# Kernel tuning notes

Measured on AMD Instinct MI355X. Metric: run time of the kernel, lower is better.

Reference implementation:

```python
import jax, jax.numpy as jnp
import numpy as np

INPUT_SIZE = 2048       # init: input_size[-1]
CONF_THRESHOLD = 0.8    # init: conf_threshold
PRED = True             # init: pred -> apply sigmoid


def setup_inputs() -> dict:
    key = jax.random.key(0)
    x = jax.random.normal(key, (1, 133, 512, 512), dtype=jnp.float32)
    return {"x": x}


def reference(x):
    # x: [1, K, H, W]
    heatmaps = jax.nn.sigmoid(x[0]) if PRED else x[0]  # [K, H, W]
    K, H, W = heatmaps.shape
    flat = heatmaps.reshape(K, H * W)
    # Fused masked-argmax over all keypoints in parallel.
    # torch.where returns row-major order, so argmax over thresholded pixels
    # equals the global argmax whenever max confidence exceeds threshold.
    idx = jnp.argmax(flat, axis=1)                      # [K]
    conf = jnp.take_along_axis(flat, idx[:, None], axis=1)[:, 0]  # [K]
    yy = (idx // W).astype(jnp.float32)
    xx = (idx % W).astype(jnp.float32)
    valid = conf > CONF_THRESHOLD                       # [K]
    joints = jnp.where(valid[:, None],
                       jnp.stack([xx, yy, conf], axis=-1),
                       jnp.float32(-1.0))               # [K, 3]
    # Original scales x,y columns for ALL rows (invalid rows become -scale).
    scale = jnp.float32(INPUT_SIZE / W)
    joints = joints.at[:, :2].multiply(scale)
    return joints
```

## Files before the change

### kernel.cpp

```cpp
#include <hip/hip_runtime.h>
#include <math.h>


#define KPTS     133
#define WW       512
#define HW       (512 * 512)
#define NCHUNK   16
#define CHUNK    (HW / NCHUNK)
#define NTHREADS 256
#define V4_PER_T (CHUNK / 4 / NTHREADS)

typedef float floatx4 __attribute__((ext_vector_type(4)));

__device__ __forceinline__ void red(float& bv, unsigned& bi, float v, unsigned i) {
    if (v > bv || (v == bv && i < bi)) { bv = v; bi = i; }
}

__global__ __launch_bounds__(NTHREADS)
void k_phase1(const float* __restrict__ x,
              float* __restrict__ pv, unsigned* __restrict__ pi) {
    const int b = blockIdx.x;
    const int k = b / NCHUNK;
    const int c = b % NCHUNK;
    const int t = threadIdx.x;

    const floatx4* src = reinterpret_cast<const floatx4*>(
        x + (size_t)k * HW + (size_t)c * CHUNK);
    const unsigned base = (unsigned)(c * CHUNK);

    float bv = -3.402823466e+38f;
    unsigned bi = 0u;

#pragma unroll
    for (int i = 0; i < V4_PER_T; ++i) {
        const int e = t + i * NTHREADS;
        const floatx4 v = __builtin_nontemporal_load(&src[e]);
        const unsigned idx = base + (unsigned)e * 4u;
        const float    m01 = fmaxf(v.x, v.y);
        const unsigned i01 = (v.x >= v.y) ? idx : idx + 1u;
        const float    m23 = fmaxf(v.z, v.w);
        const unsigned i23 = (v.z >= v.w) ? idx + 2u : idx + 3u;
        const float    m   = fmaxf(m01, m23);
        const unsigned im  = (m01 >= m23) ? i01 : i23;
        if (m > bv) { bv = m; bi = im; }
    }

    for (int off = 32; off > 0; off >>= 1) {
        const float    ov = __shfl_down(bv, off, 64);
        const unsigned oi = __shfl_down(bi, off, 64);
        red(bv, bi, ov, oi);
    }

    __shared__ float    sv[NTHREADS / 64];
    __shared__ unsigned si[NTHREADS / 64];
    const int lane = t & 63, wid = t >> 6;
    if (lane == 0) { sv[wid] = bv; si[wid] = bi; }
    __syncthreads();
    if (t == 0) {
        for (int w = 1; w < NTHREADS / 64; ++w) red(bv, bi, sv[w], si[w]);
        pv[b] = bv;
        pi[b] = bi;
    }
}

__global__ __launch_bounds__(64)
void k_phase2(const float* __restrict__ pv, const unsigned* __restrict__ pi,
              float* __restrict__ out) {
    const int k = blockIdx.x;
    const int t = threadIdx.x;

    float bv = -3.402823466e+38f;
    unsigned bi = 0xFFFFFFFFu;
    if (t < NCHUNK) { bv = pv[k * NCHUNK + t]; bi = pi[k * NCHUNK + t]; }

    for (int off = 32; off > 0; off >>= 1) {
        const float    ov = __shfl_down(bv, off, 64);
        const unsigned oi = __shfl_down(bi, off, 64);
        red(bv, bi, ov, oi);
    }

    if (t == 0) {
        const float conf = 1.0f / (1.0f + expf(-bv));
        const bool valid = conf > 0.8f;
        const float xx = (float)(bi % WW);
        const float yy = (float)(bi / WW);
        const float scale = 4.0f;
        out[k * 3 + 0] = valid ? xx * scale : -scale;
        out[k * 3 + 1] = valid ? yy * scale : -scale;
        out[k * 3 + 2] = valid ? conf : -1.0f;
    }
}

extern "C" void kernel_launch(void* const* d_in, const int* in_sizes, int n_in,
                              void* d_out, int out_size, void* d_ws, size_t ws_size,
                              hipStream_t stream) {
    const float* x = (const float*)d_in[0];
    float* out = (float*)d_out;

    float*    pv = (float*)d_ws;
    unsigned* pi = (unsigned*)((char*)d_ws + (size_t)KPTS * NCHUNK * sizeof(float));

    k_phase1<<<KPTS * NCHUNK, NTHREADS, 0, stream>>>(x, pv, pi);
    k_phase2<<<KPTS, 64, 0, stream>>>(pv, pi, out);
}
```

Baseline: 192.4 us.

## Fuse two-phase argmax into one kernel with packed 64-bit atomic max

Replaces the second reduction kernel with a packed 64-bit atomic max per keypoint, where the key is order-preserving float bits combined with the inverted index. A per-keypoint counter elects the last block to decode the result and write the output. This removes the second kernel launch and its dependency gap. In exchange it adds a memset node on the stream and atomic traffic, and it relies on the workspace being zeroed every call.

```diff
diff --git a/kernel.cpp b/kernel.cpp
--- a/kernel.cpp
+++ b/kernel.cpp
@@ -16,9 +16,16 @@
     if (v > bv || (v == bv && i < bi)) { bv = v; bi = i; }
 }
 
+__device__ __forceinline__ unsigned ord_bits(float f) {
+    const unsigned u = __float_as_uint(f);
+    return (u & 0x80000000u) ? ~u : (u | 0x80000000u);
+}
+
 __global__ __launch_bounds__(NTHREADS)
-void k_phase1(const float* __restrict__ x,
-              float* __restrict__ pv, unsigned* __restrict__ pi) {
+void k_fused(const float* __restrict__ x,
+             unsigned long long* __restrict__ amax,
+             unsigned* __restrict__ cnt,
+             float* __restrict__ out) {
     const int b = blockIdx.x;
     const int k = b / NCHUNK;
     const int c = b % NCHUNK;
@@ -56,38 +63,33 @@
     const int lane = t & 63, wid = t >> 6;
     if (lane == 0) { sv[wid] = bv; si[wid] = bi; }
     __syncthreads();
+
     if (t == 0) {
         for (int w = 1; w < NTHREADS / 64; ++w) red(bv, bi, sv[w], si[w]);
-        pv[b] = bv;
-        pi[b] = bi;
-    }
-}
 
-__global__ __launch_bounds__(64)
-void k_phase2(const float* __restrict__ pv, const unsigned* __restrict__ pi,
-              float* __restrict__ out) {
-    const int k = blockIdx.x;
-    const int t = threadIdx.x;
+        const unsigned long long key =
+            ((unsigned long long)ord_bits(bv) << 32) | (unsigned long long)(~bi);
+        __hip_atomic_fetch_max(&amax[k], key, __ATOMIC_RELEASE,
+                               __HIP_MEMORY_SCOPE_AGENT);
 
-    float bv = -3.402823466e+38f;
-    unsigned bi = 0xFFFFFFFFu;
-    if (t < NCHUNK) { bv = pv[k * NCHUNK + t]; bi = pi[k * NCHUNK + t]; }
+        const unsigned prev = __hip_atomic_fetch_add(&cnt[k], 1u, __ATOMIC_ACQ_REL,
+                                                     __HIP_MEMORY_SCOPE_AGENT);
+        if (prev == NCHUNK - 1) {
+            const unsigned long long fin =
+                __hip_atomic_load(&amax[k], __ATOMIC_ACQUIRE,
+                                  __HIP_MEMORY_SCOPE_AGENT);
+            const unsigned ob   = (unsigned)(fin >> 32);
+            const unsigned bits = (ob & 0x80000000u) ? (ob ^ 0x80000000u) : ~ob;
+            const float    val  = __uint_as_float(bits);
+            const unsigned idx  = ~(unsigned)(fin & 0xFFFFFFFFull);
 
-    for (int off = 32; off > 0; off >>= 1) {
-        const float    ov = __shfl_down(bv, off, 64);
-        const unsigned oi = __shfl_down(bi, off, 64);
-        red(bv, bi, ov, oi);
-    }
-
-    if (t == 0) {
-        const float conf = 1.0f / (1.0f + expf(-bv));
-        const bool valid = conf > 0.8f;
-        const float xx = (float)(bi % WW);
-        const float yy = (float)(bi / WW);
-        const float scale = 4.0f;
-        out[k * 3 + 0] = valid ? xx * scale : -scale;
-        out[k * 3 + 1] = valid ? yy * scale : -scale;
-        out[k * 3 + 2] = valid ? conf : -1.0f;
+            const float conf = 1.0f / (1.0f + expf(-val));
+            const bool valid = conf > 0.8f;
+            const float scale = 4.0f;
+            out[k * 3 + 0] = valid ? (float)(idx % WW) * scale : -scale;
+            out[k * 3 + 1] = valid ? (float)(idx / WW) * scale : -scale;
+            out[k * 3 + 2] = valid ? conf : -1.0f;
+        }
     }
 }
 
@@ -97,9 +99,10 @@
     const float* x = (const float*)d_in[0];
     float* out = (float*)d_out;
 
-    float*    pv = (float*)d_ws;
-    unsigned* pi = (unsigned*)((char*)d_ws + (size_t)KPTS * NCHUNK * sizeof(float));
+    unsigned long long* amax = (unsigned long long*)d_ws;
+    unsigned* cnt = (unsigned*)((char*)d_ws + KPTS * sizeof(unsigned long long));
 
-    k_phase1<<<KPTS * NCHUNK, NTHREADS, 0, stream>>>(x, pv, pi);
-    k_phase2<<<KPTS, 64, 0, stream>>>(pv, pi, out);
+    hipMemsetAsync(d_ws, 0,
+                   KPTS * (sizeof(unsigned long long) + sizeof(unsigned)), stream);
+    k_fused<<<KPTS * NCHUNK, NTHREADS, 0, stream>>>(x, amax, cnt, out);
 }
```

New measurement: 267.5 us. +39.0%, slower.

## Fuse two-phase argmax into single kernel with one 1024-thread block per keypoint

Applied to the files above, without the earlier changes.

Replaces the chunked two-kernel reduction (2128 blocks of 256 threads plus a finalize kernel) with a single kernel that gives each keypoint one 1024-thread block and writes the final joint output directly. This removes the second launch and the workspace round trip. The trade-off is only 133 blocks on a 256-CU device, so roughly half the compute units sit idle and memory bandwidth may go unused for this bandwidth-bound 140MB scan.

```diff
diff --git a/kernel.cpp b/kernel.cpp
--- a/kernel.cpp
+++ b/kernel.cpp
@@ -5,10 +5,9 @@
 #define KPTS     133
 #define WW       512
 #define HW       (512 * 512)
-#define NCHUNK   16
-#define CHUNK    (HW / NCHUNK)
-#define NTHREADS 256
-#define V4_PER_T (CHUNK / 4 / NTHREADS)
+#define NTHREADS 1024
+#define NWAVES   (NTHREADS / 64)
+#define V4_PER_T (HW / 4 / NTHREADS)
 
 typedef float floatx4 __attribute__((ext_vector_type(4)));
 
@@ -17,25 +16,20 @@
 }
 
 __global__ __launch_bounds__(NTHREADS)
-void k_phase1(const float* __restrict__ x,
-              float* __restrict__ pv, unsigned* __restrict__ pi) {
-    const int b = blockIdx.x;
-    const int k = b / NCHUNK;
-    const int c = b % NCHUNK;
+void k_rowmax(const float* __restrict__ x, float* __restrict__ out) {
+    const int k = blockIdx.x;
     const int t = threadIdx.x;
 
-    const floatx4* src = reinterpret_cast<const floatx4*>(
-        x + (size_t)k * HW + (size_t)c * CHUNK);
-    const unsigned base = (unsigned)(c * CHUNK);
+    const floatx4* src = reinterpret_cast<const floatx4*>(x + (size_t)k * HW);
 
     float bv = -3.402823466e+38f;
     unsigned bi = 0u;
 
-#pragma unroll
+#pragma unroll 8
     for (int i = 0; i < V4_PER_T; ++i) {
         const int e = t + i * NTHREADS;
         const floatx4 v = __builtin_nontemporal_load(&src[e]);
-        const unsigned idx = base + (unsigned)e * 4u;
+        const unsigned idx = (unsigned)e * 4u;
         const float    m01 = fmaxf(v.x, v.y);
         const unsigned i01 = (v.x >= v.y) ? idx : idx + 1u;
         const float    m23 = fmaxf(v.z, v.w);
@@ -51,42 +45,20 @@
         red(bv, bi, ov, oi);
     }
 
-    __shared__ float    sv[NTHREADS / 64];
-    __shared__ unsigned si[NTHREADS / 64];
+    __shared__ float    sv[NWAVES];
+    __shared__ unsigned si[NWAVES];
     const int lane = t & 63, wid = t >> 6;
     if (lane == 0) { sv[wid] = bv; si[wid] = bi; }
     __syncthreads();
-    if (t == 0) {
-        for (int w = 1; w < NTHREADS / 64; ++w) red(bv, bi, sv[w], si[w]);
-        pv[b] = bv;
-        pi[b] = bi;
-    }
-}
-
-__global__ __launch_bounds__(64)
-void k_phase2(const float* __restrict__ pv, const unsigned* __restrict__ pi,
-              float* __restrict__ out) {
-    const int k = blockIdx.x;
-    const int t = threadIdx.x;
-
-    float bv = -3.402823466e+38f;
-    unsigned bi = 0xFFFFFFFFu;
-    if (t < NCHUNK) { bv = pv[k * NCHUNK + t]; bi = pi[k * NCHUNK + t]; }
-
-    for (int off = 32; off > 0; off >>= 1) {
-        const float    ov = __shfl_down(bv, off, 64);
-        const unsigned oi = __shfl_down(bi, off, 64);
-        red(bv, bi, ov, oi);
-    }
 
     if (t == 0) {
+        for (int w = 1; w < NWAVES; ++w) red(bv, bi, sv[w], si[w]);
+
         const float conf = 1.0f / (1.0f + expf(-bv));
         const bool valid = conf > 0.8f;
-        const float xx = (float)(bi % WW);
-        const float yy = (float)(bi / WW);
         const float scale = 4.0f;
-        out[k * 3 + 0] = valid ? xx * scale : -scale;
-        out[k * 3 + 1] = valid ? yy * scale : -scale;
+        out[k * 3 + 0] = valid ? (float)(bi % WW) * scale : -scale;
+        out[k * 3 + 1] = valid ? (float)(bi / WW) * scale : -scale;
         out[k * 3 + 2] = valid ? conf : -1.0f;
     }
 }
@@ -96,10 +68,5 @@
                               hipStream_t stream) {
     const float* x = (const float*)d_in[0];
     float* out = (float*)d_out;
-
-    float*    pv = (float*)d_ws;
-    unsigned* pi = (unsigned*)((char*)d_ws + (size_t)KPTS * NCHUNK * sizeof(float));
-
-    k_phase1<<<KPTS * NCHUNK, NTHREADS, 0, stream>>>(x, pv, pi);
-    k_phase2<<<KPTS, 64, 0, stream>>>(pv, pi, out);
+    k_rowmax<<<KPTS, NTHREADS, 0, stream>>>(x, out);
 }
```

Result: slower. 203.8 us (+6.0%).
